# Kernel tuning notes

Hardware: AMD Instinct MI355X
Metric: run time of the kernel (lower is better)

## Reference

```python
import jax, jax.numpy as jnp
import numpy as np

N_NODES = 100000
N_EDGES = 3200000
D_FEAT = 512
HIDDEN = 16
N_CLASSES = 7


def _gcn_conv(x, W, b, src, dst, n_nodes):
    """PyG GCNConv (add_self_loops=True, normalize=True):
    out = D^{-1/2} (A + I) D^{-1/2} X W + b, aggregated at target nodes (dst).
    src/dst already include self loops."""
    h = x @ W  # [N, out_dim] -- transform before scatter (small message dim)
    ones = jnp.ones(dst.shape[0], dtype=x.dtype)
    deg = jax.ops.segment_sum(ones, dst, num_segments=n_nodes)  # in-degree incl. self loop
    dinv = jnp.where(deg > 0, jax.lax.rsqrt(deg), 0.0)
    norm = dinv[src] * dinv[dst]  # [E_tot]
    msg = h[src] * norm[:, None]  # gather + scale
    out = jax.ops.segment_sum(msg, dst, num_segments=n_nodes)  # scatter-add
    return out + b


def setup_inputs() -> dict:
    key = jax.random.key(0)
    k1, k2, k3, k4 = jax.random.split(key, 4)
    x = jax.random.normal(k1, (N_NODES, D_FEAT), dtype=jnp.float32)
    edge_index = jax.random.randint(k2, (2, N_EDGES), 0, N_NODES, dtype=jnp.int64)
    # Glorot-ish init for weights
    W1 = jax.random.normal(k3, (D_FEAT, HIDDEN), dtype=jnp.float32) / np.sqrt(D_FEAT)
    b1 = jnp.zeros((HIDDEN,), dtype=jnp.float32)
    W2 = jax.random.normal(k4, (HIDDEN, N_CLASSES), dtype=jnp.float32) / np.sqrt(HIDDEN)
    b2 = jnp.zeros((N_CLASSES,), dtype=jnp.float32)
    return {"x": x, "edge_index": edge_index, "W1": W1, "b1": b1, "W2": W2, "b2": b2}


def reference(x, edge_index, W1, b1, W2, b2):
    n = x.shape[0]
    loop = jnp.arange(n, dtype=edge_index.dtype)
    src = jnp.concatenate([edge_index[0], loop])  # add self loops (fixed shape)
    dst = jnp.concatenate([edge_index[1], loop])
    h = _gcn_conv(x, W1, b1, src, dst, n)
    h = jax.nn.relu(h)
    # F.dropout(training=self.training): identity in eval/inference baseline
    h = _gcn_conv(h, W2, b2, src, dst, n)
    return jax.nn.log_softmax(h, axis=1)
```

## Files before the change

kernel.cpp:

```cpp
#include <hip/hip_runtime.h>

#define NN 100000
#define NE 3200000
#define DF 512
#define HID 16
#define NC 7
#define NBK 782
#define BCAP 6144
#define GEMM_BLOCKS 1563
#define SC_B 640
#define SEDG 5000

__global__ void k_zero_i(int* __restrict__ p, int n) {
    int i = blockIdx.x * blockDim.x + threadIdx.x;
    if (i < n) p[i] = 0;
}

union SMem {
    float w[DF * HID];
    struct {
        int stage[SEDG];
        int off[783];
        int part[256];
        int cur[782];
        int gofs[782];
    } s;
};

__global__ __launch_bounds__(256) void k_fused(const float* __restrict__ x,
                                               const float* __restrict__ W1,
                                               const int* __restrict__ src,
                                               const int* __restrict__ dst,
                                               float* __restrict__ h1,
                                               int* __restrict__ bcnt,
                                               int* __restrict__ pk) {
    __shared__ SMem u;
    int tid = threadIdx.x;
    if (blockIdx.x < SC_B) {
        int* stage = u.s.stage;
        int* off   = u.s.off;
        int* part  = u.s.part;
        int* cur   = u.s.cur;
        int* gofs  = u.s.gofs;
        int e0 = blockIdx.x * SEDG;
        for (int i = tid; i < NBK; i += 256) cur[i] = 0;
        __syncthreads();
        for (int e = e0 + tid; e < e0 + SEDG; e += 256) atomicAdd(&cur[dst[e] >> 7], 1);
        __syncthreads();
        {
            int base = tid * 4;
            int sum = 0;
#pragma unroll
            for (int j = 0; j < 4; ++j) if (base + j < NBK) sum += cur[base + j];
            part[tid] = sum;
            __syncthreads();
            for (int s2 = 1; s2 < 256; s2 <<= 1) {
                int v = (tid >= s2) ? part[tid - s2] : 0;
                __syncthreads();
                part[tid] += v;
                __syncthreads();
            }
            int run = (tid > 0) ? part[tid - 1] : 0;
#pragma unroll
            for (int j = 0; j < 4; ++j) {
                int idx = base + j;
                if (idx < NBK) { off[idx] = run; run += cur[idx]; }
            }
            if (tid == 0) off[NBK] = SEDG;
        }
        __syncthreads();
        for (int i = tid; i < NBK; i += 256) {
            int h = cur[i];
            int g = h ? atomicAdd(&bcnt[i], h) : 0;
            gofs[i] = g - off[i];
            cur[i] = off[i];
        }
        __syncthreads();
        for (int e = e0 + tid; e < e0 + SEDG; e += 256) {
            int d = dst[e];
            int pos = atomicAdd(&cur[d >> 7], 1);
            stage[pos] = src[e] | ((d & 127) << 17);
        }
        __syncthreads();
        for (int i = tid; i < SEDG; i += 256) {
            int lo = 0, hi = NBK;
            while (hi - lo > 1) { int mid = (lo + hi) >> 1; if (off[mid] <= i) lo = mid; else hi = mid; }
            int idx = gofs[lo] + i;
            if (idx < BCAP) pk[(size_t)lo * BCAP + idx] = stage[i];
        }
        return;
    }
    {
        const float4* wg = (const float4*)W1;
        float4* wl = (float4*)u.w;
#pragma unroll
        for (int i = 0; i < 8; ++i) wl[tid + 256 * i] = wg[tid + 256 * i];
    }
    __syncthreads();
    int wid = (blockIdx.x - SC_B) * 4 + (tid >> 6);
    int lane = tid & 63;
    int r = lane >> 2, cc = lane & 3;
    int row = wid * 16 + r;
    if (row >= NN) return;
    const float4* xr = (const float4*)(x + (size_t)row * DF);
    const float4* wl = (const float4*)u.w;
    float4 acc = make_float4(0.f, 0.f, 0.f, 0.f);
#pragma unroll 4
    for (int i = 0; i < DF / 4; ++i) {
        float4 xv = xr[i];
        float4 w0 = wl[(4 * i + 0) * 4 + cc];
        float4 w1v = wl[(4 * i + 1) * 4 + cc];
        float4 w2 = wl[(4 * i + 2) * 4 + cc];
        float4 w3 = wl[(4 * i + 3) * 4 + cc];
        acc.x = fmaf(xv.x, w0.x, fmaf(xv.y, w1v.x, fmaf(xv.z, w2.x, fmaf(xv.w, w3.x, acc.x))));
        acc.y = fmaf(xv.x, w0.y, fmaf(xv.y, w1v.y, fmaf(xv.z, w2.y, fmaf(xv.w, w3.y, acc.y))));
        acc.z = fmaf(xv.x, w0.z, fmaf(xv.y, w1v.z, fmaf(xv.z, w2.z, fmaf(xv.w, w3.z, acc.z))));
        acc.w = fmaf(xv.x, w0.w, fmaf(xv.y, w1v.w, fmaf(xv.z, w2.w, fmaf(xv.w, w3.w, acc.w))));
    }
    *(float4*)(h1 + (size_t)row * HID + cc * 4) = acc;
}

__global__ __launch_bounds__(256) void k_sortB(const int* __restrict__ bcnt,
                                               int* __restrict__ pk,
                                               float* __restrict__ dinv,
                                               float* __restrict__ h1,
                                               int* __restrict__ ptrg,
                                               int* __restrict__ cntg) {
    __shared__ int sorted[BCAP];
    __shared__ int hist[128];
    __shared__ int off[128];
    __shared__ int cur[128];
    __shared__ float dl[128];
    int b = blockIdx.x, tid = threadIdx.x;
    if (tid < 128) hist[tid] = 0;
    __syncthreads();
    int n = min(bcnt[b], BCAP);
    int* p = pk + (size_t)b * BCAP;
    for (int i = tid; i < n; i += 256) atomicAdd(&hist[p[i] >> 17], 1);
    __syncthreads();
    if (tid < 128) off[tid] = hist[tid];
    __syncthreads();
    for (int s2 = 1; s2 < 128; s2 <<= 1) {
        int u = 0;
        if (tid < 128 && tid >= s2) u = off[tid - s2];
        __syncthreads();
        if (tid < 128) off[tid] += u;
        __syncthreads();
    }
    if (tid < 128) {
        int start = off[tid] - hist[tid];
        cur[tid] = start;
        int node = b * 128 + tid;
        float di = rsqrtf((float)hist[tid] + 1.0f);
        dl[tid] = di;
        if (node < NN) {
            dinv[node] = di;
            ptrg[node] = b * BCAP + start;
            cntg[node] = hist[tid];
        }
    }
    __syncthreads();
    for (int i = tid; i < n; i += 256) {
        int v = p[i];
        int pos = atomicAdd(&cur[v >> 17], 1);
        sorted[pos] = v & 0x1FFFF;
    }
    __syncthreads();
    for (int i = tid; i < n; i += 256) p[i] = sorted[i];
    float4* hp = (float4*)(h1 + (size_t)b * 128 * HID);
    for (int i = tid; i < 512; i += 256) {
        int ln = i >> 2;
        int node = b * 128 + ln;
        if (node < NN) {
            float di = dl[ln];
            float4 v = hp[i];
            v.x *= di; v.y *= di; v.z *= di; v.w *= di;
            hp[i] = v;
        }
    }
}

__global__ __launch_bounds__(256) void k_agg1(const int* __restrict__ ptrg,
                                              const int* __restrict__ cntg,
                                              const int* __restrict__ csr,
                                              const float* __restrict__ dinv,
                                              const float* __restrict__ h1s,
                                              const float* __restrict__ b1,
                                              const float* __restrict__ W2,
                                              float* __restrict__ h2s) {
    int tid = threadIdx.x;
    int ch = tid & 15;
    int d = blockIdx.x * 16 + (tid >> 4);
    if (d >= NN) return;
    int st = ptrg[d], n = cntg[d];
    float did = dinv[d];
    float a0 = 0.f, a1 = 0.f;
    int e = st, end = st + n;
    for (; e + 1 < end; e += 2) {
        int s0 = csr[e], s1 = csr[e + 1];
        a0 += h1s[(size_t)s0 * HID + ch];
        a1 += h1s[(size_t)s1 * HID + ch];
    }
    if (e < end) a0 += h1s[(size_t)csr[e] * HID + ch];
    float acc = (a0 + a1 + h1s[(size_t)d * HID + ch]) * did + b1[ch];
    float hr = fmaxf(acc, 0.f);
    float hj = 0.f;
#pragma unroll
    for (int k = 0; k < HID; ++k) {
        float hk = __shfl(hr, k, 16);
        if (ch < NC) hj = fmaf(hk, W2[k * NC + ch], hj);
    }
    if (ch < NC) h2s[(size_t)d * NC + ch] = hj * did;
}

__global__ __launch_bounds__(256) void k_agg2(const int* __restrict__ ptrg,
                                              const int* __restrict__ cntg,
                                              const int* __restrict__ csr,
                                              const float* __restrict__ dinv,
                                              const float* __restrict__ h2s,
                                              const float* __restrict__ b2,
                                              float* __restrict__ out) {
    int tid = threadIdx.x;
    int ch = tid & 7;
    int d = blockIdx.x * 32 + (tid >> 3);
    if (d >= NN) return;
    int st = ptrg[d], n = cntg[d];
    float did = dinv[d];
    float a0 = 0.f, a1 = 0.f;
    int e = st, end = st + n;
    for (; e + 1 < end; e += 2) {
        int s0 = csr[e], s1 = csr[e + 1];
        if (ch < NC) {
            a0 += h2s[(size_t)s0 * NC + ch];
            a1 += h2s[(size_t)s1 * NC + ch];
        }
    }
    if (e < end && ch < NC) a0 += h2s[(size_t)csr[e] * NC + ch];
    float o = -1e30f;
    if (ch < NC) o = (a0 + a1 + h2s[(size_t)d * NC + ch]) * did + b2[ch];
    float m = o;
#pragma unroll
    for (int offm = 1; offm < 8; offm <<= 1) m = fmaxf(m, __shfl_xor(m, offm, 8));
    float ex = (ch < NC) ? expf(o - m) : 0.f;
    float s8 = ex;
#pragma unroll
    for (int offm = 1; offm < 8; offm <<= 1) s8 += __shfl_xor(s8, offm, 8);
    if (ch < NC) out[(size_t)d * NC + ch] = o - m - logf(s8);
}

extern "C" void kernel_launch(void* const* d_in, const int* in_sizes, int n_in,
                              void* d_out, int out_size, void* d_ws, size_t ws_size,
                              hipStream_t stream) {
    const float* x  = (const float*)d_in[0];
    const int*   ei = (const int*)d_in[1];
    const float* W1 = (const float*)d_in[2];
    const float* b1 = (const float*)d_in[3];
    const float* W2 = (const float*)d_in[4];
    const float* b2 = (const float*)d_in[5];
    float* out = (float*)d_out;

    const int* src = ei;
    const int* dst = ei + NE;

    int*   bcnt = (int*)d_ws;
    int*   pk   = bcnt + 784;
    float* dinv = (float*)(pk + (size_t)NBK * BCAP);
    float* h1   = dinv + NN;
    float* h2   = h1 + (size_t)HID * NN;
    int*   ptrg = (int*)(h2 + (size_t)NC * NN);
    int*   cntg = ptrg + NN;

    k_zero_i<<<4, 256, 0, stream>>>(bcnt, 784);
    k_fused <<<SC_B + GEMM_BLOCKS, 256, 0, stream>>>(x, W1, src, dst, h1, bcnt, pk);
    k_sortB <<<NBK, 256, 0, stream>>>(bcnt, pk, dinv, h1, ptrg, cntg);
    k_agg1  <<<(NN + 15) / 16, 256, 0, stream>>>(ptrg, cntg, pk, dinv, h1, b1, W2, h2);
    k_agg2  <<<(NN + 31) / 32, 256, 0, stream>>>(ptrg, cntg, pk, dinv, h2, b2, out);
}
```

Baseline: 197.8 us.

## Compute one full output row per thread in GEMM with scalar W1 loads

```diff
diff --git a/kernel.cpp b/kernel.cpp
--- a/kernel.cpp
+++ b/kernel.cpp
@@ -7,24 +7,21 @@
 #define NC 7
 #define NBK 782
 #define BCAP 6144
-#define GEMM_BLOCKS 1563
 #define SC_B 640
 #define SEDG 5000
+#define GB 391
 
 __global__ void k_zero_i(int* __restrict__ p, int n) {
     int i = blockIdx.x * blockDim.x + threadIdx.x;
     if (i < n) p[i] = 0;
 }
 
-union SMem {
-    float w[DF * HID];
-    struct {
-        int stage[SEDG];
-        int off[783];
-        int part[256];
-        int cur[782];
-        int gofs[782];
-    } s;
+struct SMemScat {
+    int stage[SEDG];
+    int off[NBK + 1];
+    int part[256];
+    int cur[NBK];
+    int gofs[NBK];
 };
 
 __global__ __launch_bounds__(256) void k_fused(const float* __restrict__ x,
@@ -34,14 +31,14 @@
                                                float* __restrict__ h1,
                                                int* __restrict__ bcnt,
                                                int* __restrict__ pk) {
-    __shared__ SMem u;
+    __shared__ SMemScat u;
     int tid = threadIdx.x;
     if (blockIdx.x < SC_B) {
-        int* stage = u.s.stage;
-        int* off   = u.s.off;
-        int* part  = u.s.part;
-        int* cur   = u.s.cur;
-        int* gofs  = u.s.gofs;
+        int* stage = u.stage;
+        int* off   = u.off;
+        int* part  = u.part;
+        int* cur   = u.cur;
+        int* gofs  = u.gofs;
         int e0 = blockIdx.x * SEDG;
         for (int i = tid; i < NBK; i += 256) cur[i] = 0;
         __syncthreads();
@@ -90,34 +87,36 @@
         }
         return;
     }
-    {
-        const float4* wg = (const float4*)W1;
-        float4* wl = (float4*)u.w;
-#pragma unroll
-        for (int i = 0; i < 8; ++i) wl[tid + 256 * i] = wg[tid + 256 * i];
-    }
-    __syncthreads();
-    int wid = (blockIdx.x - SC_B) * 4 + (tid >> 6);
+    int gwave = (blockIdx.x - SC_B) * 4 + (tid >> 6);
     int lane = tid & 63;
-    int r = lane >> 2, cc = lane & 3;
-    int row = wid * 16 + r;
-    if (row >= NN) return;
-    const float4* xr = (const float4*)(x + (size_t)row * DF);
-    const float4* wl = (const float4*)u.w;
-    float4 acc = make_float4(0.f, 0.f, 0.f, 0.f);
-#pragma unroll 4
-    for (int i = 0; i < DF / 4; ++i) {
-        float4 xv = xr[i];
-        float4 w0 = wl[(4 * i + 0) * 4 + cc];
-        float4 w1v = wl[(4 * i + 1) * 4 + cc];
-        float4 w2 = wl[(4 * i + 2) * 4 + cc];
-        float4 w3 = wl[(4 * i + 3) * 4 + cc];
-        acc.x = fmaf(xv.x, w0.x, fmaf(xv.y, w1v.x, fmaf(xv.z, w2.x, fmaf(xv.w, w3.x, acc.x))));
-        acc.y = fmaf(xv.x, w0.y, fmaf(xv.y, w1v.y, fmaf(xv.z, w2.y, fmaf(xv.w, w3.y, acc.y))));
-        acc.z = fmaf(xv.x, w0.z, fmaf(xv.y, w1v.z, fmaf(xv.z, w2.z, fmaf(xv.w, w3.z, acc.z))));
-        acc.w = fmaf(xv.x, w0.w, fmaf(xv.y, w1v.w, fmaf(xv.z, w2.w, fmaf(xv.w, w3.w, acc.w))));
-    }
-    *(float4*)(h1 + (size_t)row * HID + cc * 4) = acc;
+    long row = (long)gwave * 64 + lane;
+    long crow = row < NN ? row : NN - 1;
+    const float4* xr = (const float4*)(x + crow * DF);
+    float acc[16];
+#pragma unroll
+    for (int c2 = 0; c2 < 16; ++c2) acc[c2] = 0.f;
+#pragma unroll 2
+    for (int c = 0; c < 128; ++c) {
+        float4 xv = xr[c];
+#pragma unroll
+        for (int j = 0; j < 4; ++j) {
+            float xs = (j == 0) ? xv.x : (j == 1) ? xv.y : (j == 2) ? xv.z : xv.w;
+            int k = c * 4 + j;
+#pragma unroll
+            for (int col = 0; col < 16; ++col)
+                acc[col] = fmaf(xs, W1[k * HID + col], acc[col]);
+        }
+    }
+    if (row < NN) {
+        float* hp = h1 + row * HID;
+#pragma unroll
+        for (int q = 0; q < 4; ++q) {
+            float4 o;
+            o.x = acc[q * 4 + 0]; o.y = acc[q * 4 + 1];
+            o.z = acc[q * 4 + 2]; o.w = acc[q * 4 + 3];
+            *(float4*)(hp + q * 4) = o;
+        }
+    }
 }
 
 __global__ __launch_bounds__(256) void k_sortB(const int* __restrict__ bcnt,
@@ -271,7 +270,7 @@
     int*   cntg = ptrg + NN;
 
     k_zero_i<<<4, 256, 0, stream>>>(bcnt, 784);
-    k_fused <<<SC_B + GEMM_BLOCKS, 256, 0, stream>>>(x, W1, src, dst, h1, bcnt, pk);
+    k_fused <<<SC_B + GB, 256, 0, stream>>>(x, W1, src, dst, h1, bcnt, pk);
     k_sortB <<<NBK, 256, 0, stream>>>(bcnt, pk, dinv, h1, ptrg, cntg);
     k_agg1  <<<(NN + 15) / 16, 256, 0, stream>>>(ptrg, cntg, pk, dinv, h1, b1, W2, h2);
     k_agg2  <<<(NN + 31) / 32, 256, 0, stream>>>(ptrg, cntg, pk, dinv, h2, b2, out);
```

Result: slower. 214.1 us (+8.2%).
